# Kernel optimization log

Measured on AMD Instinct MI355X. Metric: run time of the kernel, lower is better.

## Reference

```python
import jax, jax.numpy as jnp
import numpy as np

B = 128          # graphs per batch
NP = 1024        # nodes per graph
FIN = 128        # input node features
H = 128          # hidden width (SAGEConv out)
C = 10           # output classes
N = B * NP
DEG = 16
E = N * DEG
K1 = int(np.ceil(0.8 * NP))   # 820
K2 = int(np.ceil(0.8 * K1))   # 656
K3 = int(np.ceil(0.8 * K2))   # 525


def setup_inputs() -> dict:
    key = jax.random.key(0)
    k = jax.random.split(key, 16)
    x = jax.random.normal(k[0], (N, FIN), jnp.float32)
    # edges constrained within each graph (PyG batched-graph semantics)
    g = jnp.arange(E, dtype=jnp.int32) // (E // B)
    src = g * NP + jax.random.randint(k[1], (E,), 0, NP, jnp.int32)
    dst = g * NP + jax.random.randint(k[2], (E,), 0, NP, jnp.int32)
    edge_index = jnp.stack([src, dst])

    def lin(kk, o, i):
        return jax.random.normal(kk, (o, i), jnp.float32) / np.sqrt(i)

    return {
        'x': x, 'edge_index': edge_index,
        'Wl1': lin(k[3], H, FIN), 'bl1': jnp.zeros((H,), jnp.float32), 'Wr1': lin(k[4], H, FIN),
        'wp1': jax.random.normal(k[5], (H,), jnp.float32),
        'Wl2': lin(k[6], H, H), 'bl2': jnp.zeros((H,), jnp.float32), 'Wr2': lin(k[7], H, H),
        'wp2': jax.random.normal(k[8], (H,), jnp.float32),
        'Wl3': lin(k[9], H, H), 'bl3': jnp.zeros((H,), jnp.float32), 'Wr3': lin(k[10], H, H),
        'wp3': jax.random.normal(k[11], (H,), jnp.float32),
        'Wf1': lin(k[12], 64, H), 'bf1': jnp.zeros((64,), jnp.float32),
        'Wf2': lin(k[13], C, 64), 'bf2': jnp.zeros((C,), jnp.float32),
    }


def _sage(x, src, dst, em, Wl, bl, Wr):
    # PyG SAGEConv: lin_l(mean_{j in N(i)} x_j) + lin_r(x_i); edge mask em kills pruned edges
    msg = x[src] * em[:, None]                                   # [E,H] gather
    s = jax.ops.segment_sum(msg, dst, num_segments=N)            # scatter-add
    deg = jax.ops.segment_sum(em, dst, num_segments=N)
    mean = s / jnp.maximum(deg, 1.0)[:, None]
    return mean @ Wl.T + bl + x @ Wr.T


def _topk(x, w, nm, kk):
    # TopKPooling: score = x.w/||w||, keep top ceil(ratio*n) per graph, gate kept nodes by tanh(score)
    score = (x @ w) / (jnp.linalg.norm(w) + 1e-16)               # [N]
    s2 = jnp.where(nm, score, -jnp.inf).reshape(B, NP)
    _, idx = jax.lax.top_k(s2, kk)                               # [B,kk] static shape
    sel = jnp.zeros((B, NP), bool).at[jnp.arange(B)[:, None], idx].set(True).reshape(-1)
    x = jnp.where(sel[:, None], x * jnp.tanh(score)[:, None], 0.0)
    return x, sel


def _forward(x, Wl1, bl1, Wr1, wp1, Wl2, bl2, Wr2, wp2, Wl3, bl3, Wr3, wp3,
             Wf1, bf1, Wf2, bf2, edge_index):
    src, dst = edge_index[0], edge_index[1]
    nm = jnp.ones((N,), bool)                 # node alive mask
    em = jnp.ones((E,), jnp.float32)          # edge alive mask
    for (Wl, bl, Wr, wp, kk) in ((Wl1, bl1, Wr1, wp1, K1),
                                 (Wl2, bl2, Wr2, wp2, K2),
                                 (Wl3, bl3, Wr3, wp3, K3)):
        x = jax.nn.relu(_sage(x, src, dst, em, Wl, bl, Wr))
        x, nm = _topk(x, wp, nm, kk)
        em = (nm[src] & nm[dst]).astype(jnp.float32)
    # global_mean_pool over surviving nodes per graph (pruned nodes are exactly zero)
    cnt = nm.reshape(B, NP).sum(1).astype(x.dtype)
    pooled = x.reshape(B, NP, H).sum(1) / jnp.maximum(cnt, 1.0)[:, None]
    h = jax.nn.relu(pooled @ Wf1.T + bf1)
    return jax.nn.log_softmax(h @ Wf2.T + bf2, axis=-1)


def reference(x, edge_index, Wl1, bl1, Wr1, wp1, Wl2, bl2, Wr2, wp2,
              Wl3, bl3, Wr3, wp3, Wf1, bf1, Wf2, bf2):
    return _forward(x, Wl1, bl1, Wr1, wp1, Wl2, bl2, Wr2, wp2,
                    Wl3, bl3, Wr3, wp3, Wf1, bf1, Wf2, bf2, edge_index)
```

## Files before the change

kernel.cpp:

```cpp
#include <hip/hip_runtime.h>

constexpr int NGPH = 128;
constexpr int NPG  = 1024;
constexpr int NN   = NGPH * NPG;
constexpr int HD   = 128;
constexpr int EPG  = 16384;
constexpr int KS1 = 820, KS2 = 656, KS3 = 525;

typedef _Float16 half8v __attribute__((ext_vector_type(8)));
typedef float f32x4 __attribute__((ext_vector_type(4)));

__global__ __launch_bounds__(256) void init_gate(float* __restrict__ gate) {
  int i = blockIdx.x * 256 + threadIdx.x;
  if (i < NN) gate[i] = 1.0f;
}

__global__ __launch_bounds__(1024) void csr_build(int* __restrict__ ei) {
  __shared__ unsigned short sloc[EPG];
  __shared__ int cnt[NPG];
  __shared__ int scn[NPG];
  __shared__ int off[NPG];
  int g = blockIdx.x, t = threadIdx.x;
  const int* srcg = ei + (size_t)g * EPG;
  const int* dstg = ei + (size_t)NGPH * EPG + (size_t)g * EPG;
  cnt[t] = 0;
  for (int i = t; i < EPG; i += 1024)
    sloc[i] = (unsigned short)(srcg[i] - (g << 10));
  __syncthreads();
  for (int i = t; i < EPG; i += 1024)
    atomicAdd(&cnt[dstg[i] - (g << 10)], 1);
  __syncthreads();
  int* a = cnt; int* b = scn;
  for (int d = 1; d < NPG; d <<= 1) {
    b[t] = a[t] + (t >= d ? a[t - d] : 0);
    __syncthreads();
    int* tmp = a; a = b; b = tmp;
  }
  unsigned short* ssort = (unsigned short*)(ei + (size_t)g * EPG);
  unsigned short* rsout = ssort + EPG;
  int ex = t ? a[t - 1] : 0;
  rsout[t] = (unsigned short)ex;
  off[t] = ex;
  __syncthreads();
  for (int i = t; i < EPG; i += 1024) {
    int d = dstg[i] - (g << 10);
    int pos = atomicAdd(&off[d], 1);
    ssort[pos] = sloc[i];
  }
}

__global__ __launch_bounds__(256) void agg2_kernel(const float* __restrict__ X,
                                                   const int* __restrict__ ei,
                                                   const float* __restrict__ gate,
                                                   float* __restrict__ Mout) {
  int t = threadIdx.x;
  int xcd = blockIdx.x & 7, q = blockIdx.x >> 3;
  int g = ((q >> 7) << 3) + xcd;
  int r = (q & 127) * 8 + (t >> 5);
  int lane = t & 31;
  const unsigned short* ss  = (const unsigned short*)(ei + (size_t)g * EPG);
  const unsigned short* rsg = ss + EPG;
  int start = rsg[r];
  int end   = (r < 1023) ? (int)rsg[r + 1] : EPG;
  const float4* X4 = (const float4*)X;
  size_t gb4 = (size_t)(g << 10) * 32;
  float4 acc = make_float4(0.f, 0.f, 0.f, 0.f);
  float degf = 0.f;
  for (int base = start; base < end; base += 32) {
    int ec = end - base; if (ec > 32) ec = 32;
    int sl = 0; float gv = 0.f;
    if (lane < ec) {
      sl = ss[base + lane];
      gv = gate[(g << 10) + sl];
    }
    degf += (gv != 0.f) ? 1.f : 0.f;
    int e = 0;
    for (; e + 4 <= ec; e += 4) {
      int s0 = __shfl(sl, e, 32),     s1 = __shfl(sl, e + 1, 32);
      int s2 = __shfl(sl, e + 2, 32), s3 = __shfl(sl, e + 3, 32);
      float g0 = __shfl(gv, e, 32),     g1 = __shfl(gv, e + 1, 32);
      float g2 = __shfl(gv, e + 2, 32), g3 = __shfl(gv, e + 3, 32);
      float4 v0 = X4[gb4 + (size_t)s0 * 32 + lane];
      float4 v1 = X4[gb4 + (size_t)s1 * 32 + lane];
      float4 v2 = X4[gb4 + (size_t)s2 * 32 + lane];
      float4 v3 = X4[gb4 + (size_t)s3 * 32 + lane];
      acc.x += v0.x * g0 + v1.x * g1 + v2.x * g2 + v3.x * g3;
      acc.y += v0.y * g0 + v1.y * g1 + v2.y * g2 + v3.y * g3;
      acc.z += v0.z * g0 + v1.z * g1 + v2.z * g2 + v3.z * g3;
      acc.w += v0.w * g0 + v1.w * g1 + v2.w * g2 + v3.w * g3;
    }
    for (; e < ec; ++e) {
      int s0 = __shfl(sl, e, 32);
      float g0 = __shfl(gv, e, 32);
      float4 v0 = X4[gb4 + (size_t)s0 * 32 + lane];
      acc.x += v0.x * g0; acc.y += v0.y * g0;
      acc.z += v0.z * g0; acc.w += v0.w * g0;
    }
  }
#pragma unroll
  for (int m = 1; m <= 16; m <<= 1) degf += __shfl_xor(degf, m, 32);
  float inv = 1.0f / fmaxf(degf, 1.0f);
  acc.x *= inv; acc.y *= inv; acc.z *= inv; acc.w *= inv;
  ((float4*)Mout)[(size_t)((g << 10) + r) * 32 + lane] = acc;
}

constexpr int LDA = 72;
__global__ __launch_bounds__(256) void gemm_mfma(const float* S,
                                                 const float* __restrict__ X,
                                                 const float* __restrict__ Wl,
                                                 const float* __restrict__ Wr,
                                                 const float* __restrict__ bb,
                                                 const float* __restrict__ wp,
                                                 const float* __restrict__ gate,
                                                 float* Hout,
                                                 float* __restrict__ score) {
  __shared__ _Float16 Ah[128 * LDA];
  __shared__ _Float16 Al[128 * LDA];
  __shared__ _Float16 Bh[128 * LDA];
  __shared__ _Float16 Bl[128 * LDA];
  __shared__ float sc_s[128];
  int t = threadIdx.x;
  int r0 = blockIdx.x * 128;
  int lane = t & 63, wid = t >> 6;
  int wm = wid & 1, wn = wid >> 1;
  int quad = lane >> 4, mr = lane & 15;

  f32x4 acc[4][4];
#pragma unroll
  for (int i = 0; i < 4; ++i)
#pragma unroll
    for (int j = 0; j < 4; ++j) acc[i][j] = (f32x4){0.f, 0.f, 0.f, 0.f};

  for (int ks = 0; ks < 256; ks += 64) {
    bool isS = (ks < 128);
    const float* Asrc = isS ? (S + (size_t)r0 * HD + ks)
                            : (X + (size_t)r0 * HD + (ks - 128));
    const float* Wsrc = isS ? (Wl + ks) : (Wr + (ks - 128));
#pragma unroll
    for (int i = 0; i < 4; ++i) {
      int slot = t + i * 256;
      int row = slot >> 3;
      int kq = (slot & 7) * 8;
      float4 v0 = *(const float4*)&Asrc[(size_t)row * HD + kq];
      float4 v1 = *(const float4*)&Asrc[(size_t)row * HD + kq + 4];
      if (!isS) {
        float gv = gate[r0 + row];
        v0.x *= gv; v0.y *= gv; v0.z *= gv; v0.w *= gv;
        v1.x *= gv; v1.y *= gv; v1.z *= gv; v1.w *= gv;
      }
      half8v h, l;
      h[0] = (_Float16)v0.x; h[1] = (_Float16)v0.y; h[2] = (_Float16)v0.z; h[3] = (_Float16)v0.w;
      h[4] = (_Float16)v1.x; h[5] = (_Float16)v1.y; h[6] = (_Float16)v1.z; h[7] = (_Float16)v1.w;
      l[0] = (_Float16)(v0.x - (float)h[0]); l[1] = (_Float16)(v0.y - (float)h[1]);
      l[2] = (_Float16)(v0.z - (float)h[2]); l[3] = (_Float16)(v0.w - (float)h[3]);
      l[4] = (_Float16)(v1.x - (float)h[4]); l[5] = (_Float16)(v1.y - (float)h[5]);
      l[6] = (_Float16)(v1.z - (float)h[6]); l[7] = (_Float16)(v1.w - (float)h[7]);
      *(half8v*)&Ah[row * LDA + kq] = h;
      *(half8v*)&Al[row * LDA + kq] = l;
    }
#pragma unroll
    for (int i = 0; i < 4; ++i) {
      int slot = t + i * 256;
      int n = slot >> 3;
      int kq = (slot & 7) * 8;
      float4 v0 = *(const float4*)&Wsrc[(size_t)n * HD + kq];
      float4 v1 = *(const float4*)&Wsrc[(size_t)n * HD + kq + 4];
      half8v h, l;
      h[0] = (_Float16)v0.x; h[1] = (_Float16)v0.y; h[2] = (_Float16)v0.z; h[3] = (_Float16)v0.w;
      h[4] = (_Float16)v1.x; h[5] = (_Float16)v1.y; h[6] = (_Float16)v1.z; h[7] = (_Float16)v1.w;
      l[0] = (_Float16)(v0.x - (float)h[0]); l[1] = (_Float16)(v0.y - (float)h[1]);
      l[2] = (_Float16)(v0.z - (float)h[2]); l[3] = (_Float16)(v0.w - (float)h[3]);
      l[4] = (_Float16)(v1.x - (float)h[4]); l[5] = (_Float16)(v1.y - (float)h[5]);
      l[6] = (_Float16)(v1.z - (float)h[6]); l[7] = (_Float16)(v1.w - (float)h[7]);
      *(half8v*)&Bh[n * LDA + kq] = h;
      *(half8v*)&Bl[n * LDA + kq] = l;
    }
    __syncthreads();
#pragma unroll
    for (int su = 0; su < 2; ++su) {
      int ko = su * 32;
      half8v af[4], alf[4], bf[4], blf[4];
#pragma unroll
      for (int i = 0; i < 4; ++i) {
        int rowA = (wm * 64 + i * 16 + mr) * LDA + ko + quad * 8;
        af[i]  = *(const half8v*)&Ah[rowA];
        alf[i] = *(const half8v*)&Al[rowA];
      }
#pragma unroll
      for (int j = 0; j < 4; ++j) {
        int rowW = (wn * 64 + j * 16 + mr) * LDA + ko + quad * 8;
        bf[j]  = *(const half8v*)&Bh[rowW];
        blf[j] = *(const half8v*)&Bl[rowW];
      }
#pragma unroll
      for (int i = 0; i < 4; ++i)
#pragma unroll
        for (int j = 0; j < 4; ++j) {
          acc[i][j] = __builtin_amdgcn_mfma_f32_16x16x32_f16(af[i],  bf[j],  acc[i][j], 0, 0, 0);
          acc[i][j] = __builtin_amdgcn_mfma_f32_16x16x32_f16(af[i],  blf[j], acc[i][j], 0, 0, 0);
          acc[i][j] = __builtin_amdgcn_mfma_f32_16x16x32_f16(alf[i], bf[j],  acc[i][j], 0, 0, 0);
        }
    }
    __syncthreads();
  }
  if (t < 128) sc_s[t] = 0.f;
  __syncthreads();
  float p[4][4];
#pragma unroll
  for (int i = 0; i < 4; ++i)
#pragma unroll
    for (int r = 0; r < 4; ++r) p[i][r] = 0.f;
#pragma unroll
  for (int j = 0; j < 4; ++j) {
    int col = wn * 64 + j * 16 + mr;
    float bias = bb[col];
    float wv = wp[col];
#pragma unroll
    for (int i = 0; i < 4; ++i) {
      int rowg = r0 + wm * 64 + i * 16 + quad * 4;
#pragma unroll
      for (int r = 0; r < 4; ++r) {
        float ho = fmaxf(acc[i][j][r] + bias, 0.f);
        Hout[(size_t)(rowg + r) * HD + col] = ho;
        p[i][r] += ho * wv;
      }
    }
  }
#pragma unroll
  for (int i = 0; i < 4; ++i)
#pragma unroll
    for (int r = 0; r < 4; ++r) {
#pragma unroll
      for (int m = 1; m <= 8; m <<= 1) p[i][r] += __shfl_xor(p[i][r], m, 16);
      if (mr == 0) atomicAdd(&sc_s[wm * 64 + i * 16 + quad * 4 + r], p[i][r]);
    }
  __syncthreads();
  if (t < 128) score[r0 + t] = sc_s[t];
}

__global__ __launch_bounds__(256) void topk_kernel(const float* __restrict__ score,
                                                   float* __restrict__ gate,
                                                   const float* __restrict__ wp,
                                                   int kk) {
  __shared__ float sc[NPG];
  __shared__ float srt[NPG];
  __shared__ float shv[1];
  int g = blockIdx.x, t = threadIdx.x;
  if (t == 0) {
    float ss = 0.f;
    for (int i = 0; i < HD; ++i) ss += wp[i] * wp[i];
    shv[0] = 1.0f / (sqrtf(ss) + 1e-16f);
  }
  __syncthreads();
  float inv = shv[0];
#pragma unroll
  for (int q = 0; q < 4; ++q) {
    int n = t + q * 256;
    float s = score[(g << 10) + n] * inv;
    sc[n] = s;
    srt[n] = (gate[(g << 10) + n] != 0.f) ? s : -3.402823466e38f;
  }
  __syncthreads();
  for (int k2 = 2; k2 <= NPG; k2 <<= 1) {
    for (int j = k2 >> 1; j > 0; j >>= 1) {
#pragma unroll
      for (int q = 0; q < 4; ++q) {
        int i = t + q * 256;
        int l = i ^ j;
        if (l > i) {
          float a = srt[i], b = srt[l];
          if ((a > b) == ((i & k2) == 0)) { srt[i] = b; srt[l] = a; }
        }
      }
      __syncthreads();
    }
  }
  float thr = srt[NPG - kk];
#pragma unroll
  for (int q = 0; q < 4; ++q) {
    int n = t + q * 256;
    float s = sc[n];
    bool sel = (gate[(g << 10) + n] != 0.f) && (s >= thr);
    gate[(g << 10) + n] = sel ? tanhf(s) : 0.f;
  }
}

__global__ __launch_bounds__(256) void pool1_kernel(const float* __restrict__ X,
                                                    const float* __restrict__ gate,
                                                    float* __restrict__ part) {
  __shared__ float gs[128];
  __shared__ float ps[2][HD];
  int b = blockIdx.x;
  int g = b >> 3, c = b & 7;
  int t = threadIdx.x;
  if (t < 128) gs[t] = gate[(g << 10) + c * 128 + t];
  __syncthreads();
  int f = t & 127, sub = t >> 7;
  size_t base = (size_t)((g << 10) + c * 128) * HD;
  float s = 0.f;
  for (int r = sub; r < 128; r += 2)
    s += X[base + (size_t)r * HD + f] * gs[r];
  ps[sub][f] = s;
  __syncthreads();
  if (t < 128) part[(g << 10) + c * 128 + t] = ps[0][t] + ps[1][t];
}

__global__ __launch_bounds__(128) void final2_kernel(const float* __restrict__ part,
                                                     const float* __restrict__ Wf1,
                                                     const float* __restrict__ bf1,
                                                     const float* __restrict__ Wf2,
                                                     const float* __restrict__ bf2,
                                                     float* __restrict__ out) {
  __shared__ float pl[HD];
  __shared__ float h1[64];
  __shared__ float lg[10];
  __shared__ float red[2];
  int g = blockIdx.x, t = threadIdx.x;
  float tot = 0.f;
#pragma unroll
  for (int c = 0; c < 8; ++c) tot += part[(g << 10) + c * 128 + t];
  pl[t] = tot / (float)KS3;
  __syncthreads();
  if (t < 64) {
    float h = bf1[t];
    for (int ff = 0; ff < HD; ++ff) h += pl[ff] * Wf1[t * HD + ff];
    h1[t] = fmaxf(h, 0.f);
  }
  __syncthreads();
  if (t < 10) {
    float z = bf2[t];
    for (int j = 0; j < 64; ++j) z += h1[j] * Wf2[t * 64 + j];
    lg[t] = z;
  }
  __syncthreads();
  if (t == 0) {
    float m = lg[0];
    for (int cc = 1; cc < 10; ++cc) m = fmaxf(m, lg[cc]);
    float ssum = 0.f;
    for (int cc = 0; cc < 10; ++cc) ssum += expf(lg[cc] - m);
    red[0] = m; red[1] = logf(ssum);
  }
  __syncthreads();
  if (t < 10) out[g * 10 + t] = lg[t] - red[0] - red[1];
}

extern "C" void kernel_launch(void* const* d_in, const int* in_sizes, int n_in,
                              void* d_out, int out_size, void* d_ws, size_t ws_size,
                              hipStream_t stream) {
  const float* x  = (const float*)d_in[0];
  int* ei         = (int*)d_in[1];
  const float* Wl[3]  = {(const float*)d_in[2], (const float*)d_in[6],  (const float*)d_in[10]};
  const float* blv[3] = {(const float*)d_in[3], (const float*)d_in[7],  (const float*)d_in[11]};
  const float* Wr[3]  = {(const float*)d_in[4], (const float*)d_in[8],  (const float*)d_in[12]};
  const float* wp[3]  = {(const float*)d_in[5], (const float*)d_in[9],  (const float*)d_in[13]};
  const float* Wf1 = (const float*)d_in[14];
  const float* bf1 = (const float*)d_in[15];
  const float* Wf2 = (const float*)d_in[16];
  const float* bf2 = (const float*)d_in[17];
  float* out = (float*)d_out;

  float* bufA  = (float*)d_ws;
  float* bufB  = bufA + (size_t)NN * HD;
  float* gate  = bufB + (size_t)NN * HD;
  float* score = gate + NN;

  init_gate<<<NN / 256, 256, 0, stream>>>(gate);
  csr_build<<<NGPH, 1024, 0, stream>>>(ei);

  agg2_kernel<<<NN / 8, 256, 0, stream>>>(x, ei, gate, bufA);
  gemm_mfma<<<NN / 128, 256, 0, stream>>>(bufA, x, Wl[0], Wr[0], blv[0], wp[0], gate, bufA, score);
  topk_kernel<<<NGPH, 256, 0, stream>>>(score, gate, wp[0], KS1);
  agg2_kernel<<<NN / 8, 256, 0, stream>>>(bufA, ei, gate, bufB);
  gemm_mfma<<<NN / 128, 256, 0, stream>>>(bufB, bufA, Wl[1], Wr[1], blv[1], wp[1], gate, bufB, score);
  topk_kernel<<<NGPH, 256, 0, stream>>>(score, gate, wp[1], KS2);
  agg2_kernel<<<NN / 8, 256, 0, stream>>>(bufB, ei, gate, bufA);
  gemm_mfma<<<NN / 128, 256, 0, stream>>>(bufA, bufB, Wl[2], Wr[2], blv[2], wp[2], gate, bufA, score);
  topk_kernel<<<NGPH, 256, 0, stream>>>(score, gate, wp[2], KS3);

  pool1_kernel<<<NGPH * 8, 256, 0, stream>>>(bufA, gate, score);
  final2_kernel<<<NGPH, 128, 0, stream>>>(score, Wf1, bf1, Wf2, bf2, out);
}
```

Before: 572.1 us.

## Fuse neighbor mean aggregation into SAGE GEMM kernel and fold gate init into CSR build

```diff
diff --git a/kernel.cpp b/kernel.cpp
--- a/kernel.cpp
+++ b/kernel.cpp
@@ -7,15 +7,12 @@
 constexpr int EPG  = 16384;
 constexpr int KS1 = 820, KS2 = 656, KS3 = 525;
 
+typedef _Float16 half4v __attribute__((ext_vector_type(4)));
 typedef _Float16 half8v __attribute__((ext_vector_type(8)));
 typedef float f32x4 __attribute__((ext_vector_type(4)));
 
-__global__ __launch_bounds__(256) void init_gate(float* __restrict__ gate) {
-  int i = blockIdx.x * 256 + threadIdx.x;
-  if (i < NN) gate[i] = 1.0f;
-}
-
-__global__ __launch_bounds__(1024) void csr_build(int* __restrict__ ei) {
+__global__ __launch_bounds__(1024) void csr_build(int* __restrict__ ei,
+                                                  float* __restrict__ gate) {
   __shared__ unsigned short sloc[EPG];
   __shared__ int cnt[NPG];
   __shared__ int scn[NPG];
@@ -24,6 +21,7 @@
   const int* srcg = ei + (size_t)g * EPG;
   const int* dstg = ei + (size_t)NGPH * EPG + (size_t)g * EPG;
   cnt[t] = 0;
+  gate[(g << 10) + t] = 1.0f;
   for (int i = t; i < EPG; i += 1024)
     sloc[i] = (unsigned short)(srcg[i] - (g << 10));
   __syncthreads();
@@ -49,81 +47,43 @@
   }
 }
 
-__global__ __launch_bounds__(256) void agg2_kernel(const float* __restrict__ X,
-                                                   const int* __restrict__ ei,
-                                                   const float* __restrict__ gate,
-                                                   float* __restrict__ Mout) {
-  int t = threadIdx.x;
-  int xcd = blockIdx.x & 7, q = blockIdx.x >> 3;
-  int g = ((q >> 7) << 3) + xcd;
-  int r = (q & 127) * 8 + (t >> 5);
-  int lane = t & 31;
-  const unsigned short* ss  = (const unsigned short*)(ei + (size_t)g * EPG);
-  const unsigned short* rsg = ss + EPG;
-  int start = rsg[r];
-  int end   = (r < 1023) ? (int)rsg[r + 1] : EPG;
-  const float4* X4 = (const float4*)X;
-  size_t gb4 = (size_t)(g << 10) * 32;
-  float4 acc = make_float4(0.f, 0.f, 0.f, 0.f);
-  float degf = 0.f;
-  for (int base = start; base < end; base += 32) {
-    int ec = end - base; if (ec > 32) ec = 32;
-    int sl = 0; float gv = 0.f;
-    if (lane < ec) {
-      sl = ss[base + lane];
-      gv = gate[(g << 10) + sl];
-    }
-    degf += (gv != 0.f) ? 1.f : 0.f;
-    int e = 0;
-    for (; e + 4 <= ec; e += 4) {
-      int s0 = __shfl(sl, e, 32),     s1 = __shfl(sl, e + 1, 32);
-      int s2 = __shfl(sl, e + 2, 32), s3 = __shfl(sl, e + 3, 32);
-      float g0 = __shfl(gv, e, 32),     g1 = __shfl(gv, e + 1, 32);
-      float g2 = __shfl(gv, e + 2, 32), g3 = __shfl(gv, e + 3, 32);
-      float4 v0 = X4[gb4 + (size_t)s0 * 32 + lane];
-      float4 v1 = X4[gb4 + (size_t)s1 * 32 + lane];
-      float4 v2 = X4[gb4 + (size_t)s2 * 32 + lane];
-      float4 v3 = X4[gb4 + (size_t)s3 * 32 + lane];
-      acc.x += v0.x * g0 + v1.x * g1 + v2.x * g2 + v3.x * g3;
-      acc.y += v0.y * g0 + v1.y * g1 + v2.y * g2 + v3.y * g3;
-      acc.z += v0.z * g0 + v1.z * g1 + v2.z * g2 + v3.z * g3;
-      acc.w += v0.w * g0 + v1.w * g1 + v2.w * g2 + v3.w * g3;
-    }
-    for (; e < ec; ++e) {
-      int s0 = __shfl(sl, e, 32);
-      float g0 = __shfl(gv, e, 32);
-      float4 v0 = X4[gb4 + (size_t)s0 * 32 + lane];
-      acc.x += v0.x * g0; acc.y += v0.y * g0;
-      acc.z += v0.z * g0; acc.w += v0.w * g0;
-    }
-  }
-#pragma unroll
-  for (int m = 1; m <= 16; m <<= 1) degf += __shfl_xor(degf, m, 32);
-  float inv = 1.0f / fmaxf(degf, 1.0f);
-  acc.x *= inv; acc.y *= inv; acc.z *= inv; acc.w *= inv;
-  ((float4*)Mout)[(size_t)((g << 10) + r) * 32 + lane] = acc;
-}
-
 constexpr int LDA = 72;
-__global__ __launch_bounds__(256) void gemm_mfma(const float* S,
-                                                 const float* __restrict__ X,
-                                                 const float* __restrict__ Wl,
-                                                 const float* __restrict__ Wr,
-                                                 const float* __restrict__ bb,
-                                                 const float* __restrict__ wp,
-                                                 const float* __restrict__ gate,
-                                                 float* Hout,
-                                                 float* __restrict__ score) {
+__global__ __launch_bounds__(256) void sage_fused(const float* __restrict__ X,
+                                                  const int* __restrict__ ei,
+                                                  const float* __restrict__ gate,
+                                                  const float* __restrict__ Wl,
+                                                  const float* __restrict__ Wr,
+                                                  const float* __restrict__ bb,
+                                                  const float* __restrict__ wp,
+                                                  float* __restrict__ Hout,
+                                                  float* __restrict__ score) {
   __shared__ _Float16 Ah[128 * LDA];
   __shared__ _Float16 Al[128 * LDA];
   __shared__ _Float16 Bh[128 * LDA];
   __shared__ _Float16 Bl[128 * LDA];
+  __shared__ float gate_s[NPG];
   __shared__ float sc_s[128];
   int t = threadIdx.x;
-  int r0 = blockIdx.x * 128;
+  int xcd = blockIdx.x & 7;
+  int local = blockIdx.x >> 3;
+  int g = xcd * 16 + (local >> 3);
+  int m128 = (local & 7) * 128;
+  int gb = g << 10;
+  int gbm = gb + m128;
   int lane = t & 63, wid = t >> 6;
   int wm = wid & 1, wn = wid >> 1;
   int quad = lane >> 4, mr = lane & 15;
+  int gr = t >> 5, lane32 = t & 31;
+  int f4 = lane32 & 15, e2 = lane32 >> 4;
+
+  const unsigned short* ss  = (const unsigned short*)(ei + (size_t)g * EPG);
+  const unsigned short* rsg = ss + EPG;
+  const float4* X4 = (const float4*)X;
+  size_t gb4 = (size_t)gb * 32;
+
+#pragma unroll
+  for (int i = 0; i < 4; ++i) gate_s[t + i * 256] = gate[gb + t + i * 256];
+  __syncthreads();
 
   f32x4 acc[4][4];
 #pragma unroll
@@ -131,33 +91,10 @@
 #pragma unroll
     for (int j = 0; j < 4; ++j) acc[i][j] = (f32x4){0.f, 0.f, 0.f, 0.f};
 
-  for (int ks = 0; ks < 256; ks += 64) {
-    bool isS = (ks < 128);
-    const float* Asrc = isS ? (S + (size_t)r0 * HD + ks)
-                            : (X + (size_t)r0 * HD + (ks - 128));
-    const float* Wsrc = isS ? (Wl + ks) : (Wr + (ks - 128));
-#pragma unroll
-    for (int i = 0; i < 4; ++i) {
-      int slot = t + i * 256;
-      int row = slot >> 3;
-      int kq = (slot & 7) * 8;
-      float4 v0 = *(const float4*)&Asrc[(size_t)row * HD + kq];
-      float4 v1 = *(const float4*)&Asrc[(size_t)row * HD + kq + 4];
-      if (!isS) {
-        float gv = gate[r0 + row];
-        v0.x *= gv; v0.y *= gv; v0.z *= gv; v0.w *= gv;
-        v1.x *= gv; v1.y *= gv; v1.z *= gv; v1.w *= gv;
-      }
-      half8v h, l;
-      h[0] = (_Float16)v0.x; h[1] = (_Float16)v0.y; h[2] = (_Float16)v0.z; h[3] = (_Float16)v0.w;
-      h[4] = (_Float16)v1.x; h[5] = (_Float16)v1.y; h[6] = (_Float16)v1.z; h[7] = (_Float16)v1.w;
-      l[0] = (_Float16)(v0.x - (float)h[0]); l[1] = (_Float16)(v0.y - (float)h[1]);
-      l[2] = (_Float16)(v0.z - (float)h[2]); l[3] = (_Float16)(v0.w - (float)h[3]);
-      l[4] = (_Float16)(v1.x - (float)h[4]); l[5] = (_Float16)(v1.y - (float)h[5]);
-      l[6] = (_Float16)(v1.z - (float)h[6]); l[7] = (_Float16)(v1.w - (float)h[7]);
-      *(half8v*)&Ah[row * LDA + kq] = h;
-      *(half8v*)&Al[row * LDA + kq] = l;
-    }
+  for (int ki = 0; ki < 4; ++ki) {
+    int kt = (ki + 2) & 3;
+    int ko = (kt & 1) * 64;
+    const float* Wsrc = (kt < 2) ? (Wl + ko) : (Wr + ko);
 #pragma unroll
     for (int i = 0; i < 4; ++i) {
       int slot = t + i * 256;
@@ -175,20 +112,103 @@
       *(half8v*)&Bh[n * LDA + kq] = h;
       *(half8v*)&Bl[n * LDA + kq] = l;
     }
+    if (kt >= 2) {
+#pragma unroll
+      for (int i = 0; i < 4; ++i) {
+        int slot = t + i * 256;
+        int row = slot >> 3;
+        int kq = (slot & 7) * 8;
+        const float* Asrc = &X[(size_t)(gbm + row) * HD + ko];
+        float4 v0 = *(const float4*)&Asrc[kq];
+        float4 v1 = *(const float4*)&Asrc[kq + 4];
+        float gv = gate_s[m128 + row];
+        v0.x *= gv; v0.y *= gv; v0.z *= gv; v0.w *= gv;
+        v1.x *= gv; v1.y *= gv; v1.z *= gv; v1.w *= gv;
+        half8v h, l;
+        h[0] = (_Float16)v0.x; h[1] = (_Float16)v0.y; h[2] = (_Float16)v0.z; h[3] = (_Float16)v0.w;
+        h[4] = (_Float16)v1.x; h[5] = (_Float16)v1.y; h[6] = (_Float16)v1.z; h[7] = (_Float16)v1.w;
+        l[0] = (_Float16)(v0.x - (float)h[0]); l[1] = (_Float16)(v0.y - (float)h[1]);
+        l[2] = (_Float16)(v0.z - (float)h[2]); l[3] = (_Float16)(v0.w - (float)h[3]);
+        l[4] = (_Float16)(v1.x - (float)h[4]); l[5] = (_Float16)(v1.y - (float)h[5]);
+        l[6] = (_Float16)(v1.z - (float)h[6]); l[7] = (_Float16)(v1.w - (float)h[7]);
+        *(half8v*)&Ah[row * LDA + kq] = h;
+        *(half8v*)&Al[row * LDA + kq] = l;
+      }
+    } else {
+      int kt16 = (kt & 1) * 16;
+      for (int rr = 0; rr < 16; ++rr) {
+        int rloc = gr * 16 + rr;
+        int rg = m128 + rloc;
+        int start = rsg[rg];
+        int end = (rg < 1023) ? (int)rsg[rg + 1] : EPG;
+        float4 a = make_float4(0.f, 0.f, 0.f, 0.f);
+        float degf = 0.f;
+        for (int base = start; base < end; base += 32) {
+          int ec = end - base; if (ec > 32) ec = 32;
+          int sl = 0; float gv = 0.f;
+          if (lane32 < ec) { sl = ss[base + lane32]; gv = gate_s[sl]; }
+          degf += (gv != 0.f) ? 1.f : 0.f;
+          int e = 0;
+          for (; e + 8 <= ec; e += 8) {
+            int s0 = __shfl(sl, e + e2, 32),     s1 = __shfl(sl, e + 2 + e2, 32);
+            int s2 = __shfl(sl, e + 4 + e2, 32), s3 = __shfl(sl, e + 6 + e2, 32);
+            float g0 = __shfl(gv, e + e2, 32),     g1 = __shfl(gv, e + 2 + e2, 32);
+            float g2 = __shfl(gv, e + 4 + e2, 32), g3 = __shfl(gv, e + 6 + e2, 32);
+            float4 v0 = X4[gb4 + (size_t)s0 * 32 + kt16 + f4];
+            float4 v1 = X4[gb4 + (size_t)s1 * 32 + kt16 + f4];
+            float4 v2 = X4[gb4 + (size_t)s2 * 32 + kt16 + f4];
+            float4 v3 = X4[gb4 + (size_t)s3 * 32 + kt16 + f4];
+            a.x += v0.x * g0 + v1.x * g1 + v2.x * g2 + v3.x * g3;
+            a.y += v0.y * g0 + v1.y * g1 + v2.y * g2 + v3.y * g3;
+            a.z += v0.z * g0 + v1.z * g1 + v2.z * g2 + v3.z * g3;
+            a.w += v0.w * g0 + v1.w * g1 + v2.w * g2 + v3.w * g3;
+          }
+          for (; e + 2 <= ec; e += 2) {
+            int s0 = __shfl(sl, e + e2, 32);
+            float g0 = __shfl(gv, e + e2, 32);
+            float4 v0 = X4[gb4 + (size_t)s0 * 32 + kt16 + f4];
+            a.x += v0.x * g0; a.y += v0.y * g0;
+            a.z += v0.z * g0; a.w += v0.w * g0;
+          }
+          if (e < ec) {
+            int s0 = __shfl(sl, e, 32);
+            float g0 = __shfl(gv, e, 32);
+            if (e2 == 0) {
+              float4 v0 = X4[gb4 + (size_t)s0 * 32 + kt16 + f4];
+              a.x += v0.x * g0; a.y += v0.y * g0;
+              a.z += v0.z * g0; a.w += v0.w * g0;
+            }
+          }
+        }
+        a.x += __shfl_xor(a.x, 16, 32); a.y += __shfl_xor(a.y, 16, 32);
+        a.z += __shfl_xor(a.z, 16, 32); a.w += __shfl_xor(a.w, 16, 32);
+#pragma unroll
+        for (int mm = 1; mm <= 16; mm <<= 1) degf += __shfl_xor(degf, mm, 32);
+        float dinv = 1.0f / fmaxf(degf, 1.0f);
+        a.x *= dinv; a.y *= dinv; a.z *= dinv; a.w *= dinv;
+        half4v h, l;
+        h[0] = (_Float16)a.x; h[1] = (_Float16)a.y;
+        h[2] = (_Float16)a.z; h[3] = (_Float16)a.w;
+        l[0] = (_Float16)(a.x - (float)h[0]); l[1] = (_Float16)(a.y - (float)h[1]);
+        l[2] = (_Float16)(a.z - (float)h[2]); l[3] = (_Float16)(a.w - (float)h[3]);
+        if (e2 == 0) *(half4v*)&Ah[rloc * LDA + f4 * 4] = h;
+        else         *(half4v*)&Al[rloc * LDA + f4 * 4] = l;
+      }
+    }
     __syncthreads();
 #pragma unroll
     for (int su = 0; su < 2; ++su) {
-      int ko = su * 32;
+      int so = su * 32;
       half8v af[4], alf[4], bf[4], blf[4];
 #pragma unroll
       for (int i = 0; i < 4; ++i) {
-        int rowA = (wm * 64 + i * 16 + mr) * LDA + ko + quad * 8;
+        int rowA = (wm * 64 + i * 16 + mr) * LDA + so + quad * 8;
         af[i]  = *(const half8v*)&Ah[rowA];
         alf[i] = *(const half8v*)&Al[rowA];
       }
 #pragma unroll
       for (int j = 0; j < 4; ++j) {
-        int rowW = (wn * 64 + j * 16 + mr) * LDA + ko + quad * 8;
+        int rowW = (wn * 64 + j * 16 + mr) * LDA + so + quad * 8;
         bf[j]  = *(const half8v*)&Bh[rowW];
         blf[j] = *(const half8v*)&Bl[rowW];
       }
@@ -217,7 +237,7 @@
     float wv = wp[col];
 #pragma unroll
     for (int i = 0; i < 4; ++i) {
-      int rowg = r0 + wm * 64 + i * 16 + quad * 4;
+      int rowg = gbm + wm * 64 + i * 16 + quad * 4;
 #pragma unroll
       for (int r = 0; r < 4; ++r) {
         float ho = fmaxf(acc[i][j][r] + bias, 0.f);
@@ -231,11 +251,11 @@
 #pragma unroll
     for (int r = 0; r < 4; ++r) {
 #pragma unroll
-      for (int m = 1; m <= 8; m <<= 1) p[i][r] += __shfl_xor(p[i][r], m, 16);
+      for (int mm = 1; mm <= 8; mm <<= 1) p[i][r] += __shfl_xor(p[i][r], mm, 16);
       if (mr == 0) atomicAdd(&sc_s[wm * 64 + i * 16 + quad * 4 + r], p[i][r]);
     }
   __syncthreads();
-  if (t < 128) score[r0 + t] = sc_s[t];
+  if (t < 128) score[gbm + t] = sc_s[t];
 }
 
 __global__ __launch_bounds__(256) void topk_kernel(const float* __restrict__ score,
@@ -364,17 +384,13 @@
   float* gate  = bufB + (size_t)NN * HD;
   float* score = gate + NN;
 
-  init_gate<<<NN / 256, 256, 0, stream>>>(gate);
-  csr_build<<<NGPH, 1024, 0, stream>>>(ei);
-
-  agg2_kernel<<<NN / 8, 256, 0, stream>>>(x, ei, gate, bufA);
-  gemm_mfma<<<NN / 128, 256, 0, stream>>>(bufA, x, Wl[0], Wr[0], blv[0], wp[0], gate, bufA, score);
+  csr_build<<<NGPH, 1024, 0, stream>>>(ei, gate);
+
+  sage_fused<<<1024, 256, 0, stream>>>(x, ei, gate, Wl[0], Wr[0], blv[0], wp[0], bufA, score);
   topk_kernel<<<NGPH, 256, 0, stream>>>(score, gate, wp[0], KS1);
-  agg2_kernel<<<NN / 8, 256, 0, stream>>>(bufA, ei, gate, bufB);
-  gemm_mfma<<<NN / 128, 256, 0, stream>>>(bufB, bufA, Wl[1], Wr[1], blv[1], wp[1], gate, bufB, score);
+  sage_fused<<<1024, 256, 0, stream>>>(bufA, ei, gate, Wl[1], Wr[1], blv[1], wp[1], bufB, score);
   topk_kernel<<<NGPH, 256, 0, stream>>>(score, gate, wp[1], KS2);
-  agg2_kernel<<<NN / 8, 256, 0, stream>>>(bufB, ei, gate, bufA);
-  gemm_mfma<<<NN / 128, 256, 0, stream>>>(bufA, bufB, Wl[2], Wr[2], blv[2], wp[2], gate, bufA, score);
+  sage_fused<<<1024, 256, 0, stream>>>(bufB, ei, gate, Wl[2], Wr[2], blv[2], wp[2], bufA, score);
   topk_kernel<<<NGPH, 256, 0, stream>>>(score, gate, wp[2], KS3);
 
   pool1_kernel<<<NGPH * 8, 256, 0, stream>>>(bufA, gate, score);
```

Measured after the change: 740.2 us. 1.29x slower.
